# Optimization experiments

Hardware: AMD Instinct MI355X
Metric: run time of the kernel (lower is better)

The kernel has to match this reference:

```python
import jax, jax.numpy as jnp
import numpy as np

FUT_LEN = 12
OBS_LEN = 8
N_COORD = 2
HIDDEN = 128  # z_dim + s_dim = 64 + 64
N_AGENTS = 131072


def setup_inputs() -> dict:
    key = jax.random.key(0)
    ks = jax.random.split(key, 9)
    H, C = HIDDEN, N_COORD
    return {
        "obs_traj_rel": jax.random.normal(ks[0], (OBS_LEN, N_AGENTS, C), jnp.float32),
        "fut_traj_rel": jax.random.normal(ks[1], (FUT_LEN, N_AGENTS, C), jnp.float32),
        "pred_lstm_hidden": jax.random.normal(ks[2], (N_AGENTS, H), jnp.float32),
        # LSTMCell params (PyTorch layout: [4H, in] / [4H, H], gate order i,f,g,o)
        "W_ih": 0.1 * jax.random.normal(ks[3], (4 * H, C), jnp.float32),
        "W_hh": 0.1 * jax.random.normal(ks[4], (4 * H, H), jnp.float32),
        "b_ih": jnp.zeros((4 * H,), jnp.float32),
        "b_hh": jnp.zeros((4 * H,), jnp.float32),
        # hidden2pos Linear
        "W_out": 0.1 * jax.random.normal(ks[5], (C, H), jnp.float32),
        "b_out": jnp.zeros((C,), jnp.float32),
    }


def reference(obs_traj_rel, fut_traj_rel, pred_lstm_hidden,
              W_ih, W_hh, b_ih, b_hh, W_out, b_out):
    H = pred_lstm_hidden.shape[-1]
    x0 = obs_traj_rel[OBS_LEN - 1, :, :N_COORD]           # [N, 2]
    c0 = jnp.zeros_like(pred_lstm_hidden)                  # [N, H]

    def step(carry, _):
        h, c, x = carry
        gates = x @ W_ih.T + b_ih + h @ W_hh.T + b_hh      # [N, 4H]
        i, f, g, o = jnp.split(gates, 4, axis=-1)          # PyTorch gate order
        c_new = jax.nn.sigmoid(f) * c + jax.nn.sigmoid(i) * jnp.tanh(g)
        h_new = jax.nn.sigmoid(o) * jnp.tanh(c_new)
        out = h_new @ W_out.T + b_out                      # [N, 2]
        return (h_new, c_new, out), out

    _, outs = jax.lax.scan(step, (pred_lstm_hidden, c0, x0), None, length=FUT_LEN)
    return outs  # [fut_len, N, 2]
```

## Files before the change

### kernel.cpp

```cpp
#include <hip/hip_runtime.h>

typedef unsigned short u16;
typedef __attribute__((ext_vector_type(8))) short short8;
typedef __attribute__((ext_vector_type(4))) float f32x4;
typedef __attribute__((ext_vector_type(2))) float f32x2;

#define N_AGENTS 131072
#define HID 128
#define FUT 12
#define OBS 8

constexpr int AG = 16;
#define NEG_K  (-1.4426950408889634f)
#define NEG_2K (-2.8853900817779268f)

__device__ __forceinline__ u16 f2bf(float f) {
    union { float f; unsigned int i; } v; v.f = f;
    unsigned int u = v.i;
    return (u16)((u + 0x7fffu + ((u >> 16) & 1u)) >> 16);
}
__device__ __forceinline__ float bexp2(float x) {
#if __has_builtin(__builtin_amdgcn_exp2f)
    return __builtin_amdgcn_exp2f(x);
#else
    float r; asm("v_exp_f32 %0, %1" : "=v"(r) : "v"(x)); return r;
#endif
}
__device__ __forceinline__ float brcp(float x) {
#if __has_builtin(__builtin_amdgcn_rcpf)
    return __builtin_amdgcn_rcpf(x);
#else
    float r; asm("v_rcp_f32 %0, %1" : "=v"(r) : "v"(x)); return r;
#endif
}
__device__ __forceinline__ unsigned cvtpk(float lo, float hi) {
    unsigned r; asm("v_cvt_pk_bf16_f32 %0, %1, %2" : "=v"(r) : "v"(lo), "v"(hi)); return r;
}

__launch_bounds__(1024, 4)
__global__ void lstm_dec_kernel(const float* __restrict__ obs,
                                const float* __restrict__ h0g,
                                const float* __restrict__ Wih,
                                const float* __restrict__ Whh,
                                const float* __restrict__ bih,
                                const float* __restrict__ bhh,
                                const float* __restrict__ Wout,
                                const float* __restrict__ bout,
                                float* __restrict__ dout)
{
    __shared__ short8 wB[32][4][64];
    __shared__ short8 hb[2][32][17];
    __shared__ short8 outb_lds[4][64];
    __shared__ float  xt[32][2];
    __shared__ float  ot[FUT][32][2];

    const int tid  = threadIdx.x;
    const int lane = tid & 63;
    const int wv   = tid >> 6;
    const int at   = wv & 1;
    const int hs   = wv >> 1;
    const int r    = lane & 15;
    const int kb   = lane >> 4;

    const float bout0 = bout[0];
    const float bout1 = bout[1];
    const float bo_sc = (r == 0) ? bout0 : ((r == 1) ? bout1 : 0.0f);
    const f32x4 oInit = {bo_sc, bo_sc, bo_sc, bo_sc};

    float beff[4];
#pragma unroll
    for (int nt = 0; nt < 4; ++nt) {
        const float gs = (nt == 2) ? NEG_2K : NEG_K;
        int c = nt * HID + hs * 16 + r;
        float w0 = Wih[c * 2 + 0];
        float w1 = Wih[c * 2 + 1];
        beff[nt] = (bih[c] + bhh[c] + w0 * bout0 + w1 * bout1) * gs;
    }

    if (at == 0) {
#pragma unroll
        for (int kf = 0; kf < 4; ++kf) {
            const int k0 = kf * 32 + kb * 8;
            float wo0[8], wo1[8];
#pragma unroll
            for (int j = 0; j < 8; ++j) {
                wo0[j] = Wout[0 * HID + k0 + j];
                wo1[j] = Wout[1 * HID + k0 + j];
            }
#pragma unroll
            for (int nt = 0; nt < 4; ++nt) {
                const float gs = (nt == 2) ? NEG_2K : NEG_K;
                int c = nt * HID + hs * 16 + r;
                float s0 = Wih[c * 2 + 0] * gs;
                float s1 = Wih[c * 2 + 1] * gs;
                short8 tt;
#pragma unroll
                for (int j = 0; j < 8; ++j) {
                    float f = Whh[(size_t)c * HID + k0 + j] * gs
                            + s0 * wo0[j] + s1 * wo1[j];
                    tt[j] = (short)f2bf(f);
                }
                wB[nt * 8 + hs][kf][lane] = tt;
            }
        }
    }
    if (wv == 1) {
#pragma unroll
        for (int kf = 0; kf < 4; ++kf) {
            const int k0 = kf * 32 + kb * 8;
            short8 ob;
#pragma unroll
            for (int j = 0; j < 8; ++j) {
                float sel = (r == 0) ? Wout[k0 + j]
                          : ((r == 1) ? Wout[HID + k0 + j] : 0.0f);
                ob[j] = (short)f2bf(sel);
            }
            outb_lds[kf][lane] = ob;
        }
    }

#define GATES(rb)                                                    \
    _Pragma("unroll")                                                \
    for (int kf = 0; kf < 4; ++kf)                                   \
        af[kf] = hb[rb][at * 16 + r][kf * 4 + kb];                   \
    {                                                                \
        const f32x4 z4 = {0.f, 0.f, 0.f, 0.f};                       \
        _Pragma("unroll")                                            \
        for (int nt = 0; nt < 4; ++nt)                               \
            acc[nt] = __builtin_amdgcn_mfma_f32_16x16x32_bf16(       \
                af[0], wB[nt * 8 + hs][0][lane], z4, 0, 0, 0);       \
        _Pragma("unroll")                                            \
        for (int kf = 1; kf < 4; ++kf)                               \
            _Pragma("unroll")                                        \
            for (int nt = 0; nt < 4; ++nt)                           \
                acc[nt] = __builtin_amdgcn_mfma_f32_16x16x32_bf16(   \
                    af[kf], wB[nt * 8 + hs][kf][lane], acc[nt], 0, 0, 0); \
    }

#define OUT_TILE(rb, dst_expr)                                       \
    if (wv < 2) {                                                    \
        short8 t0 = hb[rb][at * 16 + r][kb];                         \
        f32x4 oacc = __builtin_amdgcn_mfma_f32_16x16x32_bf16(        \
            t0, outb_lds[0][lane], oInit, 0, 0, 0);                  \
        t0 = hb[rb][at * 16 + r][4 + kb];                            \
        oacc = __builtin_amdgcn_mfma_f32_16x16x32_bf16(              \
            t0, outb_lds[1][lane], oacc, 0, 0, 0);                   \
        t0 = hb[rb][at * 16 + r][8 + kb];                            \
        oacc = __builtin_amdgcn_mfma_f32_16x16x32_bf16(              \
            t0, outb_lds[2][lane], oacc, 0, 0, 0);                   \
        t0 = hb[rb][at * 16 + r][12 + kb];                           \
        oacc = __builtin_amdgcn_mfma_f32_16x16x32_bf16(              \
            t0, outb_lds[3][lane], oacc, 0, 0, 0);                   \
        if (r < 2) {                                                 \
            _Pragma("unroll")                                        \
            for (int q = 0; q < 4; ++q)                              \
                (dst_expr)[at * 16 + kb * 4 + q][r] = oacc[q];       \
        }                                                            \
    }

#define CORR()                                                       \
    {                                                                \
        float dx0[4], dx1[4];                                        \
        _Pragma("unroll")                                            \
        for (int q = 0; q < 4; ++q) {                                \
            int a  = at * 16 + kb * 4 + q;                           \
            int ag = A0 + a;                                         \
            dx0[q] = obs[((size_t)(OBS - 1) * N_AGENTS + ag) * 2 + 0] - xt[a][0]; \
            dx1[q] = obs[((size_t)(OBS - 1) * N_AGENTS + ag) * 2 + 1] - xt[a][1]; \
        }                                                            \
        _Pragma("unroll")                                            \
        for (int nt = 0; nt < 4; ++nt) {                             \
            const float gs = (nt == 2) ? NEG_2K : NEG_K;             \
            int c = nt * HID + hs * 16 + r;                          \
            float w0s = Wih[c * 2 + 0] * gs;                         \
            float w1s = Wih[c * 2 + 1] * gs;                         \
            _Pragma("unroll")                                        \
            for (int q = 0; q < 4; ++q)                              \
                acc[nt][q] += dx0[q] * w0s + dx1[q] * w1s;           \
        }                                                            \
    }

#define CELLP(qa, qb)                                                \
    {                                                                \
        f32x2 Ei = {bexp2(acc[0][qa] + beff[0]), bexp2(acc[0][qb] + beff[0])}; \
        f32x2 Ef = {bexp2(acc[1][qa] + beff[1]), bexp2(acc[1][qb] + beff[1])}; \
        f32x2 Gg = {bexp2(acc[2][qa] + beff[2]), bexp2(acc[2][qb] + beff[2])}; \
        f32x2 Eo = {bexp2(acc[3][qa] + beff[3]), bexp2(acc[3][qb] + beff[3])}; \
        f32x2 c2 = {cf[qa], cf[qb]};                                 \
        f32x2 t1 = 1.0f + Ei;                                        \
        f32x2 t2 = 1.0f + Gg;                                        \
        f32x2 t3 = 1.0f + Ef;                                        \
        f32x2 t12 = t1 * t2;                                         \
        f32x2 num = t12 * c2 + t3 * (1.0f - Gg);                     \
        f32x2 den = t12 * t3;                                        \
        f32x2 R1 = {brcp(den.x), brcp(den.y)};                       \
        f32x2 cn = num * R1;                                         \
        cf[qa] = cn.x; cf[qb] = cn.y;                                \
        f32x2 ga = NEG_2K * cn;                                      \
        f32x2 Gc = {bexp2(ga.x), bexp2(ga.y)};                       \
        f32x2 u1 = (1.0f + Eo) * (1.0f + Gc);                        \
        f32x2 R2 = {brcp(u1.x), brcp(u1.y)};                         \
        f32x2 hv = (1.0f - Gc) * R2;                                 \
        unsigned pk = cvtpk(hv.x, hv.y);                             \
        hbase[(at * 16 + kb * 4 + qa) * 136 + hs * 16 + r] = (u16)pk; \
        hbase[(at * 16 + kb * 4 + qb) * 136 + hs * 16 + r] = (u16)(pk >> 16); \
    }

#define ACTIV(wb)                                                    \
    {                                                                \
        u16* hbase = (u16*)&hb[wb][0][0];                            \
        CELLP(0, 1) CELLP(2, 3)                                      \
    }

#pragma unroll 1
    for (int t = 0; t < AG; ++t) {
        const int A0 = (blockIdx.x * AG + t) * 32;

        {
            int row = tid >> 5;
            int c4  = (tid & 31) * 4;
            const float* hp = h0g + (size_t)(A0 + row) * HID + c4;
            f32x4 v = *(const f32x4*)hp;
            unsigned* dst = (unsigned*)&hb[1][row][0] + (tid & 31) * 2;
            dst[0] = cvtpk(v[0], v[1]);
            dst[1] = cvtpk(v[2], v[3]);
        }
        f32x4 cf = {0.f, 0.f, 0.f, 0.f};
        f32x4 acc[4];
        short8 af[4];
        __syncthreads();

        GATES(1)
        OUT_TILE(1, xt)
        __syncthreads();
        CORR()
        ACTIV(0)
        __syncthreads();

#pragma unroll 1
        for (int s = 1; s < FUT; ++s) {
            const int rb = (s - 1) & 1;
            GATES(rb)
            OUT_TILE(rb, ot[s - 1])
            ACTIV(s & 1)
            __syncthreads();
        }

        OUT_TILE(1, ot[FUT - 1])
        __syncthreads();

        if (tid < FUT * 64) {
            const float* otf = &ot[0][0][0];
            dout[((size_t)(tid >> 6) * N_AGENTS + A0) * 2 + (tid & 63)] = otf[tid];
        }
    }
#undef GATES
#undef OUT_TILE
#undef CORR
#undef CELLP
#undef ACTIV
}

extern "C" void kernel_launch(void* const* d_in, const int* in_sizes, int n_in,
                              void* d_out, int out_size, void* d_ws, size_t ws_size,
                              hipStream_t stream) {
    const float* obs  = (const float*)d_in[0];
    const float* h0   = (const float*)d_in[2];
    const float* Wih  = (const float*)d_in[3];
    const float* Whh  = (const float*)d_in[4];
    const float* bih  = (const float*)d_in[5];
    const float* bhh  = (const float*)d_in[6];
    const float* Wout = (const float*)d_in[7];
    const float* bo   = (const float*)d_in[8];
    float* out = (float*)d_out;

    dim3 grid(N_AGENTS / (AG * 32));
    lstm_dec_kernel<<<grid, 1024, 0, stream>>>(obs, h0, Wih, Whh, bih, bhh, Wout, bo, out);
}
```

Measured before the change: 321.9 us.

## Process 64 agents per block with two MFMA tiles per wave sharing weight loads

Each block now handles 64 agents per inner iteration instead of 32. Each wave computes two 16-agent tiles against the same weight fragments, so every B-operand LDS read is reused across two MFMAs. The double-buffered hidden state becomes a single buffer, with an extra barrier between the gate and activation phases. Weight preparation is spread across all 16 waves instead of 8, and the grid and agents-per-block loop are rescaled to match. The trade-off is more registers per wave and one extra __syncthreads per step.

```diff
diff --git a/kernel.cpp b/kernel.cpp
--- a/kernel.cpp
+++ b/kernel.cpp
@@ -10,7 +10,7 @@
 #define FUT 12
 #define OBS 8
 
-constexpr int AG = 16;
+constexpr int AG = 8;
 #define NEG_K  (-1.4426950408889634f)
 #define NEG_2K (-2.8853900817779268f)
 
@@ -49,16 +49,18 @@
                                 float* __restrict__ dout)
 {
     __shared__ short8 wB[32][4][64];
-    __shared__ short8 hb[2][32][17];
+    __shared__ short8 hb[64][17];
     __shared__ short8 outb_lds[4][64];
-    __shared__ float  xt[32][2];
-    __shared__ float  ot[FUT][32][2];
+    __shared__ float  xt[64][2];
+    __shared__ float  ot[FUT][64][2];
 
     const int tid  = threadIdx.x;
     const int lane = tid & 63;
     const int wv   = tid >> 6;
-    const int at   = wv & 1;
-    const int hs   = wv >> 1;
+    const int hs   = wv & 7;
+    const int ap   = wv >> 3;
+    const int T0   = ap * 2;
+    const int T1   = ap * 2 + 1;
     const int r    = lane & 15;
     const int kb   = lane >> 4;
 
@@ -72,39 +74,31 @@
     for (int nt = 0; nt < 4; ++nt) {
         const float gs = (nt == 2) ? NEG_2K : NEG_K;
         int c = nt * HID + hs * 16 + r;
-        float w0 = Wih[c * 2 + 0];
-        float w1 = Wih[c * 2 + 1];
-        beff[nt] = (bih[c] + bhh[c] + w0 * bout0 + w1 * bout1) * gs;
-    }
-
-    if (at == 0) {
+        beff[nt] = (bih[c] + bhh[c] + Wih[c * 2 + 0] * bout0 + Wih[c * 2 + 1] * bout1) * gs;
+    }
+
+#pragma unroll
+    for (int ci = 0; ci < 2; ++ci) {
+        const int ct  = wv * 2 + ci;
+        const int nt  = ct >> 3;
+        const float gs = (nt == 2) ? NEG_2K : NEG_K;
+        const int c   = nt * HID + (ct & 7) * 16 + r;
+        const float s0 = Wih[c * 2 + 0] * gs;
+        const float s1 = Wih[c * 2 + 1] * gs;
 #pragma unroll
         for (int kf = 0; kf < 4; ++kf) {
             const int k0 = kf * 32 + kb * 8;
-            float wo0[8], wo1[8];
+            short8 tt;
 #pragma unroll
             for (int j = 0; j < 8; ++j) {
-                wo0[j] = Wout[0 * HID + k0 + j];
-                wo1[j] = Wout[1 * HID + k0 + j];
+                float f = Whh[(size_t)c * HID + k0 + j] * gs
+                        + s0 * Wout[k0 + j] + s1 * Wout[HID + k0 + j];
+                tt[j] = (short)f2bf(f);
             }
-#pragma unroll
-            for (int nt = 0; nt < 4; ++nt) {
-                const float gs = (nt == 2) ? NEG_2K : NEG_K;
-                int c = nt * HID + hs * 16 + r;
-                float s0 = Wih[c * 2 + 0] * gs;
-                float s1 = Wih[c * 2 + 1] * gs;
-                short8 tt;
-#pragma unroll
-                for (int j = 0; j < 8; ++j) {
-                    float f = Whh[(size_t)c * HID + k0 + j] * gs
-                            + s0 * wo0[j] + s1 * wo1[j];
-                    tt[j] = (short)f2bf(f);
-                }
-                wB[nt * 8 + hs][kf][lane] = tt;
-            }
-        }
-    }
-    if (wv == 1) {
+            wB[ct][kf][lane] = tt;
+        }
+    }
+    if (wv == 15) {
 #pragma unroll
         for (int kf = 0; kf < 4; ++kf) {
             const int k0 = kf * 32 + kb * 8;
@@ -119,54 +113,63 @@
         }
     }
 
-#define GATES(rb)                                                    \
-    _Pragma("unroll")                                                \
-    for (int kf = 0; kf < 4; ++kf)                                   \
-        af[kf] = hb[rb][at * 16 + r][kf * 4 + kb];                   \
-    {                                                                \
+#define GATES()                                                      \
+    {                                                                \
+        short8 a0[4], a1[4];                                         \
+        _Pragma("unroll")                                            \
+        for (int kf = 0; kf < 4; ++kf) {                             \
+            a0[kf] = hb[T0 * 16 + r][kf * 4 + kb];                   \
+            a1[kf] = hb[T1 * 16 + r][kf * 4 + kb];                   \
+        }                                                            \
         const f32x4 z4 = {0.f, 0.f, 0.f, 0.f};                       \
         _Pragma("unroll")                                            \
-        for (int nt = 0; nt < 4; ++nt)                               \
-            acc[nt] = __builtin_amdgcn_mfma_f32_16x16x32_bf16(       \
-                af[0], wB[nt * 8 + hs][0][lane], z4, 0, 0, 0);       \
+        for (int nt = 0; nt < 4; ++nt) {                             \
+            short8 b = wB[nt * 8 + hs][0][lane];                     \
+            accA[nt] = __builtin_amdgcn_mfma_f32_16x16x32_bf16(a0[0], b, z4, 0, 0, 0); \
+            accB[nt] = __builtin_amdgcn_mfma_f32_16x16x32_bf16(a1[0], b, z4, 0, 0, 0); \
+        }                                                            \
         _Pragma("unroll")                                            \
         for (int kf = 1; kf < 4; ++kf)                               \
             _Pragma("unroll")                                        \
-            for (int nt = 0; nt < 4; ++nt)                           \
-                acc[nt] = __builtin_amdgcn_mfma_f32_16x16x32_bf16(   \
-                    af[kf], wB[nt * 8 + hs][kf][lane], acc[nt], 0, 0, 0); \
-    }
-
-#define OUT_TILE(rb, dst_expr)                                       \
-    if (wv < 2) {                                                    \
-        short8 t0 = hb[rb][at * 16 + r][kb];                         \
+            for (int nt = 0; nt < 4; ++nt) {                         \
+                short8 b = wB[nt * 8 + hs][kf][lane];                \
+                accA[nt] = __builtin_amdgcn_mfma_f32_16x16x32_bf16(a0[kf], b, accA[nt], 0, 0, 0); \
+                accB[nt] = __builtin_amdgcn_mfma_f32_16x16x32_bf16(a1[kf], b, accB[nt], 0, 0, 0); \
+            }                                                        \
+    }
+
+#define OUT_TILE(dst_expr)                                           \
+    if (wv < 4) {                                                    \
+        short8 t0 = hb[wv * 16 + r][kb];                             \
         f32x4 oacc = __builtin_amdgcn_mfma_f32_16x16x32_bf16(        \
             t0, outb_lds[0][lane], oInit, 0, 0, 0);                  \
-        t0 = hb[rb][at * 16 + r][4 + kb];                            \
+        t0 = hb[wv * 16 + r][4 + kb];                                \
         oacc = __builtin_amdgcn_mfma_f32_16x16x32_bf16(              \
             t0, outb_lds[1][lane], oacc, 0, 0, 0);                   \
-        t0 = hb[rb][at * 16 + r][8 + kb];                            \
+        t0 = hb[wv * 16 + r][8 + kb];                                \
         oacc = __builtin_amdgcn_mfma_f32_16x16x32_bf16(              \
             t0, outb_lds[2][lane], oacc, 0, 0, 0);                   \
-        t0 = hb[rb][at * 16 + r][12 + kb];                           \
+        t0 = hb[wv * 16 + r][12 + kb];                               \
         oacc = __builtin_amdgcn_mfma_f32_16x16x32_bf16(              \
             t0, outb_lds[3][lane], oacc, 0, 0, 0);                   \
         if (r < 2) {                                                 \
             _Pragma("unroll")                                        \
             for (int q = 0; q < 4; ++q)                              \
-                (dst_expr)[at * 16 + kb * 4 + q][r] = oacc[q];       \
+                (dst_expr)[wv * 16 + kb * 4 + q][r] = oacc[q];       \
         }                                                            \
     }
 
 #define CORR()                                                       \
     {                                                                \
-        float dx0[4], dx1[4];                                        \
+        float dA0[4], dA1[4], dB0[4], dB1[4];                        \
         _Pragma("unroll")                                            \
         for (int q = 0; q < 4; ++q) {                                \
-            int a  = at * 16 + kb * 4 + q;                           \
-            int ag = A0 + a;                                         \
-            dx0[q] = obs[((size_t)(OBS - 1) * N_AGENTS + ag) * 2 + 0] - xt[a][0]; \
-            dx1[q] = obs[((size_t)(OBS - 1) * N_AGENTS + ag) * 2 + 1] - xt[a][1]; \
+            int aA = T0 * 16 + kb * 4 + q;                           \
+            int aB = T1 * 16 + kb * 4 + q;                           \
+            dA0[q] = obs[((size_t)(OBS - 1) * N_AGENTS + A0 + aA) * 2 + 0] - xt[aA][0]; \
+            dA1[q] = obs[((size_t)(OBS - 1) * N_AGENTS + A0 + aA) * 2 + 1] - xt[aA][1]; \
+            dB0[q] = obs[((size_t)(OBS - 1) * N_AGENTS + A0 + aB) * 2 + 0] - xt[aB][0]; \
+            dB1[q] = obs[((size_t)(OBS - 1) * N_AGENTS + A0 + aB) * 2 + 1] - xt[aB][1]; \
         }                                                            \
         _Pragma("unroll")                                            \
         for (int nt = 0; nt < 4; ++nt) {                             \
@@ -175,12 +178,14 @@
             float w0s = Wih[c * 2 + 0] * gs;                         \
             float w1s = Wih[c * 2 + 1] * gs;                         \
             _Pragma("unroll")                                        \
-            for (int q = 0; q < 4; ++q)                              \
-                acc[nt][q] += dx0[q] * w0s + dx1[q] * w1s;           \
-        }                                                            \
-    }
-
-#define CELLP(qa, qb)                                                \
+            for (int q = 0; q < 4; ++q) {                            \
+                accA[nt][q] += dA0[q] * w0s + dA1[q] * w1s;          \
+                accB[nt][q] += dB0[q] * w0s + dB1[q] * w1s;          \
+            }                                                        \
+        }                                                            \
+    }
+
+#define CELLP(acc, cf, qa, qb, T)                                    \
     {                                                                \
         f32x2 Ei = {bexp2(acc[0][qa] + beff[0]), bexp2(acc[0][qb] + beff[0])}; \
         f32x2 Ef = {bexp2(acc[1][qa] + beff[1]), bexp2(acc[1][qb] + beff[1])}; \
@@ -202,56 +207,66 @@
         f32x2 R2 = {brcp(u1.x), brcp(u1.y)};                         \
         f32x2 hv = (1.0f - Gc) * R2;                                 \
         unsigned pk = cvtpk(hv.x, hv.y);                             \
-        hbase[(at * 16 + kb * 4 + qa) * 136 + hs * 16 + r] = (u16)pk; \
-        hbase[(at * 16 + kb * 4 + qb) * 136 + hs * 16 + r] = (u16)(pk >> 16); \
-    }
-
-#define ACTIV(wb)                                                    \
-    {                                                                \
-        u16* hbase = (u16*)&hb[wb][0][0];                            \
-        CELLP(0, 1) CELLP(2, 3)                                      \
+        hbase[((T) * 16 + kb * 4 + qa) * 136 + hcol] = (u16)pk;      \
+        hbase[((T) * 16 + kb * 4 + qb) * 136 + hcol] = (u16)(pk >> 16); \
+    }
+
+#define ACTIV()                                                      \
+    {                                                                \
+        u16* hbase = (u16*)&hb[0][0];                                \
+        const int hcol = hs * 16 + r;                                \
+        CELLP(accA, cfA, 0, 1, T0) CELLP(accA, cfA, 2, 3, T0)        \
+        CELLP(accB, cfB, 0, 1, T1) CELLP(accB, cfB, 2, 3, T1)        \
     }
 
 #pragma unroll 1
     for (int t = 0; t < AG; ++t) {
-        const int A0 = (blockIdx.x * AG + t) * 32;
+        const int A0 = (blockIdx.x * AG + t) * 64;
 
         {
-            int row = tid >> 5;
-            int c4  = (tid & 31) * 4;
-            const float* hp = h0g + (size_t)(A0 + row) * HID + c4;
-            f32x4 v = *(const f32x4*)hp;
-            unsigned* dst = (unsigned*)&hb[1][row][0] + (tid & 31) * 2;
-            dst[0] = cvtpk(v[0], v[1]);
-            dst[1] = cvtpk(v[2], v[3]);
-        }
-        f32x4 cf = {0.f, 0.f, 0.f, 0.f};
-        f32x4 acc[4];
-        short8 af[4];
-        __syncthreads();
-
-        GATES(1)
-        OUT_TILE(1, xt)
+            int row = tid >> 4;
+            int c8  = (tid & 15) * 8;
+            const float* hp = h0g + (size_t)(A0 + row) * HID + c8;
+            f32x4 lo = *(const f32x4*)hp;
+            f32x4 hi = *(const f32x4*)(hp + 4);
+            short8 a;
+            unsigned* apk = (unsigned*)&a;
+            apk[0] = cvtpk(lo[0], lo[1]);
+            apk[1] = cvtpk(lo[2], lo[3]);
+            apk[2] = cvtpk(hi[0], hi[1]);
+            apk[3] = cvtpk(hi[2], hi[3]);
+            hb[row][tid & 15] = a;
+        }
+        f32x4 cfA = {0.f, 0.f, 0.f, 0.f};
+        f32x4 cfB = {0.f, 0.f, 0.f, 0.f};
+        f32x4 accA[4], accB[4];
+        __syncthreads();
+
+        GATES()
+        OUT_TILE(xt)
         __syncthreads();
         CORR()
-        ACTIV(0)
+        ACTIV()
         __syncthreads();
 
 #pragma unroll 1
         for (int s = 1; s < FUT; ++s) {
-            const int rb = (s - 1) & 1;
-            GATES(rb)
-            OUT_TILE(rb, ot[s - 1])
-            ACTIV(s & 1)
+            GATES()
+            OUT_TILE(ot[s - 1])
             __syncthreads();
-        }
-
-        OUT_TILE(1, ot[FUT - 1])
-        __syncthreads();
-
-        if (tid < FUT * 64) {
+            ACTIV()
+            __syncthreads();
+        }
+
+        OUT_TILE(ot[FUT - 1])
+        __syncthreads();
+
+        {
             const float* otf = &ot[0][0][0];
-            dout[((size_t)(tid >> 6) * N_AGENTS + A0) * 2 + (tid & 63)] = otf[tid];
+            dout[((size_t)(tid >> 7) * N_AGENTS + A0) * 2 + (tid & 127)] = otf[tid];
+            int idx = tid + 1024;
+            if (idx < FUT * 128)
+                dout[((size_t)(idx >> 7) * N_AGENTS + A0) * 2 + (idx & 127)] = otf[idx];
         }
     }
 #undef GATES
@@ -274,6 +289,6 @@
     const float* bo   = (const float*)d_in[8];
     float* out = (float*)d_out;
 
-    dim3 grid(N_AGENTS / (AG * 32));
+    dim3 grid(N_AGENTS / (AG * 64));
     lstm_dec_kernel<<<grid, 1024, 0, stream>>>(obs, h0, Wih, Whh, bih, bhh, Wout, bo, out);
 }
```

Result: faster. 303.1 us (-5.8%).
